# Kernel tuning notes

Hardware: AMD Instinct MI355X
Metric: run time of the kernel (lower is better)

The kernel has to match this reference:

```python
import jax, jax.numpy as jnp
import numpy as np

D = 1024       # d_model
H = 16         # nhead
HD = D // H    # head_dim = 64
FF = 4096      # dim_feedforward
EPS = 1e-5


def layer_norm(x, gamma, beta, eps=EPS):
    mu = jnp.mean(x, axis=-1, keepdims=True)
    var = jnp.var(x, axis=-1, keepdims=True)
    return (x - mu) * jax.lax.rsqrt(var + eps) * gamma + beta


def setup_inputs() -> dict:
    key = jax.random.key(0)
    ks = jax.random.split(key, 12)
    rn = lambda k, shape, s=0.02: (jax.random.normal(k, shape, jnp.float32) * s)
    return {
        "src": jax.random.normal(ks[0], (4, 2048, D), jnp.float32),
        "Wqkv": rn(ks[1], (D, 3 * D)),          # qkv_proj weight (bias=False), stored (in,out)
        "Wout": rn(ks[2], (D, D)),              # out_proj weight (bias=False)
        "W1": rn(ks[3], (D, FF)),               # linear1
        "b1": jnp.zeros((FF,), jnp.float32),
        "W2": rn(ks[4], (FF, D)),               # linear2
        "b2": jnp.zeros((D,), jnp.float32),
        "g1": jnp.ones((D,), jnp.float32),      # norm1 weight
        "be1": jnp.zeros((D,), jnp.float32),    # norm1 bias
        "g2": jnp.ones((D,), jnp.float32),      # norm2 weight
        "be2": jnp.zeros((D,), jnp.float32),    # norm2 bias
    }


def reference(src, Wqkv, Wout, W1, b1, W2, b2, g1, be1, g2, be2):
    B, S, _ = src.shape
    # --- self attention (naive/MATH-backend SDPA, post-norm, eval: dropout=0) ---
    qkv = src @ Wqkv                                  # [B,S,3D]
    qkv = qkv.reshape(B, S, 3, H, HD)
    q = qkv[:, :, 0].transpose(0, 2, 1, 3)            # [B,H,S,HD]
    k = qkv[:, :, 1].transpose(0, 2, 1, 3)
    v = qkv[:, :, 2].transpose(0, 2, 1, 3)
    scores = jnp.einsum("bhqd,bhkd->bhqk", q, k) / np.float32(np.sqrt(HD))  # [B,H,S,S]
    attn = jax.nn.softmax(scores, axis=-1)
    ctx = jnp.einsum("bhqk,bhkd->bhqd", attn, v)      # [B,H,S,HD]
    ctx = ctx.transpose(0, 2, 1, 3).reshape(B, S, D)  # [B,S,D]
    attn_out = ctx @ Wout
    # residual + norm1
    x = layer_norm(src + attn_out, g1, be1)
    # --- FFN ---
    ff = jax.nn.relu(x @ W1 + b1) @ W2 + b2
    # residual + norm2
    return layer_norm(x + ff, g2, be2)
```

## Files before the change

kernel.cpp:

```cpp
#include <hip/hip_runtime.h>
#include <hip/hip_bf16.h>


typedef __attribute__((ext_vector_type(8))) short          short8;
typedef __attribute__((ext_vector_type(8))) unsigned short ushort8;
typedef __attribute__((ext_vector_type(4))) float          f32x4;
typedef __attribute__((ext_vector_type(2))) unsigned int   uivec2;

__device__ __forceinline__ unsigned short f2bf(float f) {
    union { float f; unsigned int u; } v; v.f = f;
    unsigned int u = v.u;
    unsigned int r = (u + 0x7fffu + ((u >> 16) & 1u)) >> 16;
    return (unsigned short)r;
}

__device__ __forceinline__ float bf2f(unsigned short u) {
    union { unsigned int u; float f; } v; v.u = ((unsigned int)u) << 16;
    return v.f;
}

__device__ __forceinline__ unsigned int pack_bf16_trunc(float lo, float hi) {
    union { float f; unsigned int u; } a, b; a.f = lo; b.f = hi;
    return __builtin_amdgcn_perm(b.u, a.u, 0x07060302u);
}

__device__ __forceinline__ void async_load16(const void* g, void* l) {
    __builtin_amdgcn_global_load_lds(
        (const __attribute__((address_space(1))) void*)(unsigned long long)g,
        (__attribute__((address_space(3))) void*)(unsigned long long)l,
        16, 0, 0);
}

__device__ __forceinline__ void softmax_frag(const f32x4* s,
                                             short8& pf0, short8& pf1) {
    unsigned int aw[4], bw[4];
#pragma unroll
    for (int nt = 0; nt < 4; nt++) {
        float p0 = __builtin_amdgcn_exp2f(s[nt][0]);
        float p1 = __builtin_amdgcn_exp2f(s[nt][1]);
        float p2 = __builtin_amdgcn_exp2f(s[nt][2]);
        float p3 = __builtin_amdgcn_exp2f(s[nt][3]);
        aw[nt] = pack_bf16_trunc(p0, p1);
        bw[nt] = pack_bf16_trunc(p2, p3);
    }
    uivec2 rA = __builtin_amdgcn_permlane32_swap(aw[0], aw[1], false, false);
    uivec2 sA = __builtin_amdgcn_permlane32_swap(aw[2], aw[3], false, false);
    uivec2 rB = __builtin_amdgcn_permlane32_swap(bw[0], bw[1], false, false);
    uivec2 sB = __builtin_amdgcn_permlane32_swap(bw[2], bw[3], false, false);
    uivec2 tA = __builtin_amdgcn_permlane16_swap(rA.x, rA.y, false, false);
    uivec2 uA = __builtin_amdgcn_permlane16_swap(sA.x, sA.y, false, false);
    uivec2 tB = __builtin_amdgcn_permlane16_swap(rB.x, rB.y, false, false);
    uivec2 uB = __builtin_amdgcn_permlane16_swap(sB.x, sB.y, false, false);
    union { unsigned int w[4]; short8 v; } P0, P1;
    P0.w[0] = tA.x; P0.w[1] = tB.x; P0.w[2] = tA.y; P0.w[3] = tB.y;
    P1.w[0] = uA.x; P1.w[1] = uB.x; P1.w[2] = uA.y; P1.w[3] = uB.y;
    pf0 = P0.v;
    pf1 = P1.v;
}

__global__ __launch_bounds__(256) void cast_bf16_kernel(
    const float* __restrict__ x, unsigned short* __restrict__ y) {
    size_t i = ((size_t)blockIdx.x * 256 + threadIdx.x) * 4;
    float4 v = *(const float4*)(x + i);
    ushort4 o; o.x = f2bf(v.x); o.y = f2bf(v.y); o.z = f2bf(v.z); o.w = f2bf(v.w);
    *(ushort4*)(y + i) = o;
}

__global__ __launch_bounds__(256) void transpose_cast_kernel(
    const float* __restrict__ W, unsigned short* __restrict__ Wt, int K, int N) {
    __shared__ float tile[32][33];
    int n0 = blockIdx.x * 32, k0 = blockIdx.y * 32;
    int tx = threadIdx.x & 31, ty = threadIdx.x >> 5;
#pragma unroll
    for (int i = 0; i < 32; i += 8)
        tile[ty + i][tx] = W[(size_t)(k0 + ty + i) * N + n0 + tx];
    __syncthreads();
#pragma unroll
    for (int i = 0; i < 32; i += 8)
        Wt[(size_t)(n0 + ty + i) * K + k0 + tx] = f2bf(tile[tx][ty + i]);
}

template <int MODE>
__global__ __launch_bounds__(256) void gemm_bf16_kernel(
    const unsigned short* __restrict__ A, const unsigned short* __restrict__ Bt,
    int M, int N, int K, int Kstride,
    float* __restrict__ outF, unsigned short* __restrict__ outB,
    const float* __restrict__ bias,
    const float* __restrict__ resF, const unsigned short* __restrict__ resB,
    unsigned short* __restrict__ vtB) {
    __shared__ unsigned short As[2][128 * 32];
    __shared__ unsigned short Bs[2][128 * 32];

    const int t = threadIdx.x;
    const int m0 = blockIdx.x * 128, n0 = blockIdx.y * 128;
    const int koff = blockIdx.z * K;
    const int wid = t >> 6, lane = t & 63;
    const int wm = wid >> 1, wn = wid & 1;
    const int lr = lane & 15, quad = lane >> 4;

    const int srow = lane >> 2;
    const int sch  = ((lane & 3) ^ (srow & 3)) * 8;
    const unsigned short* Ag =
        A  + (size_t)(m0 + wid * 32 + srow) * Kstride + koff + sch;
    const unsigned short* Bg =
        Bt + (size_t)(n0 + wid * 32 + srow) * Kstride + koff + sch;
    const int wofs = (wid * 32) * 32;
    const size_t rstep = (size_t)16 * Kstride;

    const int axs = ((quad ^ (lr & 3))) * 8;
    f32x4 acc[4][4] = {};

    const int nK = K >> 5;
    async_load16(Ag,         &As[0][wofs]);
    async_load16(Ag + rstep, &As[0][wofs + 16 * 32]);
    async_load16(Bg,         &Bs[0][wofs]);
    async_load16(Bg + rstep, &Bs[0][wofs + 16 * 32]);

    for (int kt = 0; kt < nK; kt++) {
        const int cur = kt & 1, nxt = cur ^ 1;
        __syncthreads();
        if (kt + 1 < nK) {
            const int k1 = (kt + 1) * 32;
            async_load16(Ag + k1,         &As[nxt][wofs]);
            async_load16(Ag + k1 + rstep, &As[nxt][wofs + 16 * 32]);
            async_load16(Bg + k1,         &Bs[nxt][wofs]);
            async_load16(Bg + k1 + rstep, &Bs[nxt][wofs + 16 * 32]);
        }

        short8 af[4], bfr[4];
#pragma unroll
        for (int i = 0; i < 4; i++) {
            af[i]  = *(const short8*)&As[cur][(wm * 64 + i * 16 + lr) * 32 + axs];
            bfr[i] = *(const short8*)&Bs[cur][(wn * 64 + i * 16 + lr) * 32 + axs];
        }
#pragma unroll
        for (int mi = 0; mi < 4; mi++)
#pragma unroll
            for (int ni = 0; ni < 4; ni++)
                acc[mi][ni] = __builtin_amdgcn_mfma_f32_16x16x32_bf16(
                    af[mi], bfr[ni], acc[mi][ni], 0, 0, 0);
    }

    const float QSC = 0.18033688011112042f;
    float* pOut = (MODE == 5) ? outF + (size_t)blockIdx.z * M * N : outF;
    unsigned short* pOutB =
        (MODE == 8) ? outB + (size_t)blockIdx.z * M * N : outB;
#pragma unroll
    for (int mi = 0; mi < 4; mi++)
#pragma unroll
        for (int ni = 0; ni < 4; ni++) {
            const int col  = n0 + wn * 64 + ni * 16 + lr;
            const int row0 = m0 + wm * 64 + mi * 16 + quad * 4;
            if (MODE == 4 && col >= 2048) {
                int bb = row0 >> 11, ss = row0 & 2047, c = col - 2048;
                ushort4 ov;
                ov.x = f2bf(acc[mi][ni][0]); ov.y = f2bf(acc[mi][ni][1]);
                ov.z = f2bf(acc[mi][ni][2]); ov.w = f2bf(acc[mi][ni][3]);
                *(ushort4*)&vtB[((size_t)bb * 1024 + c) * 2048 + ss] = ov;
            } else {
#pragma unroll
                for (int r = 0; r < 4; r++) {
                    size_t idx = (size_t)(row0 + r) * N + col;
                    float v = acc[mi][ni][r];
                    if (MODE == 4) {
                        outB[idx] = f2bf(col < 1024 ? v * QSC : v);
                    } else if (MODE == 0) {
                        outB[idx] = f2bf(v);
                    } else if (MODE == 1) {
                        outF[idx] = v + resF[idx];
                    } else if (MODE == 2) {
                        v += bias[col];
                        outB[idx] = f2bf(v > 0.f ? v : 0.f);
                    } else if (MODE == 3) {
                        outF[idx] = v + bias[col] + bf2f(resB[idx]);
                    } else if (MODE == 7) {
                        outB[idx] = f2bf(v + bf2f(resB[idx]));
                    } else if (MODE == 8) {
                        pOutB[idx] = f2bf(v);
                    } else {
                        pOut[idx] = v;
                    }
                }
            }
        }
}

__global__ __launch_bounds__(256, 4) void attention_kernel(
    const unsigned short* __restrict__ qkv, const unsigned short* __restrict__ Vt,
    unsigned short* __restrict__ ctx) {
    __shared__ unsigned short Kbuf[2][64 * 64];
    __shared__ unsigned short Vbuf[2][64 * 64];

    const int qt = blockIdx.x, h = blockIdx.y, b = blockIdx.z;
    const int t = threadIdx.x, wid = t >> 6, lane = t & 63;
    const int lr = lane & 15, quad = lane >> 4;
    const int q0 = qt * 128 + wid * 32;

    size_t qbaseA = ((size_t)(b * 2048 + q0 + lr)) * 3072 + h * 64;
    size_t qbaseB = ((size_t)(b * 2048 + q0 + 16 + lr)) * 3072 + h * 64;
    short8 qfA0 = *(const short8*)(qkv + qbaseA + quad * 8);
    short8 qfA1 = *(const short8*)(qkv + qbaseA + 32 + quad * 8);
    short8 qfB0 = *(const short8*)(qkv + qbaseB + quad * 8);
    short8 qfB1 = *(const short8*)(qkv + qbaseB + 32 + quad * 8);

    const int srow = wid * 8 + (lane >> 3);
    const int sch  = ((lane & 7) ^ (srow & 7)) * 8;
    const unsigned short* Kg =
        qkv + (size_t)b * 2048 * 3072 + 1024 + h * 64 + (size_t)srow * 3072 + sch;
    const unsigned short* Vg =
        Vt + ((size_t)b * 1024 + h * 64 + srow) * 2048 + sch;
    unsigned short* KsB = (unsigned short*)&Kbuf[0][(wid * 8) * 64];
    unsigned short* VsB = (unsigned short*)&Vbuf[0][(wid * 8) * 64];
    const int bufstep = 64 * 64;

    short8 ones;
#pragma unroll
    for (int i = 0; i < 8; i++) ones[i] = (short)0x3F80;

    f32x4 oA[4] = {}, oB[4] = {};
    f32x4 laccA = {}, laccB = {};

#pragma unroll
    for (int half = 0; half < 2; half++) {
        async_load16(Kg + (size_t)(half * 32) * 3072, KsB + half * 32 * 64);
        async_load16(Vg + (size_t)(half * 32) * 2048, VsB + half * 32 * 64);
    }

    const int swz = lr & 7;

    for (int kt = 0; kt < 32; kt++) {
        const int cur = kt & 1, nxt = cur ^ 1;
        __syncthreads();
        if (kt + 1 < 32) {
#pragma unroll
            for (int half = 0; half < 2; half++) {
                async_load16(Kg + (size_t)((kt + 1) * 64 + half * 32) * 3072,
                             KsB + nxt * bufstep + half * 32 * 64);
                async_load16(Vg + (size_t)(half * 32) * 2048 + (kt + 1) * 64,
                             VsB + nxt * bufstep + half * 32 * 64);
            }
        }

        const unsigned short* Kc = &Kbuf[cur][0];
        const unsigned short* Vc = &Vbuf[cur][0];

        f32x4 sA[4] = {}, sB[4] = {};
#pragma unroll
        for (int nt = 0; nt < 4; nt++) {
            const unsigned short* krow = Kc + (nt * 16 + lr) * 64;
            short8 kf0 = *(const short8*)(krow + (quad ^ swz) * 8);
            short8 kf1 = *(const short8*)(krow + ((quad + 4) ^ swz) * 8);
            sA[nt] = __builtin_amdgcn_mfma_f32_16x16x32_bf16(kf0, qfA0, sA[nt], 0, 0, 0);
            sA[nt] = __builtin_amdgcn_mfma_f32_16x16x32_bf16(kf1, qfA1, sA[nt], 0, 0, 0);
            sB[nt] = __builtin_amdgcn_mfma_f32_16x16x32_bf16(kf0, qfB0, sB[nt], 0, 0, 0);
            sB[nt] = __builtin_amdgcn_mfma_f32_16x16x32_bf16(kf1, qfB1, sB[nt], 0, 0, 0);
        }

        short8 pfA0, pfA1, pfB0, pfB1;
        softmax_frag(sA, pfA0, pfA1);
        softmax_frag(sB, pfB0, pfB1);

#pragma unroll
        for (int nt = 0; nt < 4; nt++) {
            const unsigned short* vrow = Vc + (nt * 16 + lr) * 64;
            short8 vf0 = *(const short8*)(vrow + (quad ^ swz) * 8);
            short8 vf1 = *(const short8*)(vrow + ((quad + 4) ^ swz) * 8);
            oA[nt] = __builtin_amdgcn_mfma_f32_16x16x32_bf16(pfA0, vf0, oA[nt], 0, 0, 0);
            oA[nt] = __builtin_amdgcn_mfma_f32_16x16x32_bf16(pfA1, vf1, oA[nt], 0, 0, 0);
            oB[nt] = __builtin_amdgcn_mfma_f32_16x16x32_bf16(pfB0, vf0, oB[nt], 0, 0, 0);
            oB[nt] = __builtin_amdgcn_mfma_f32_16x16x32_bf16(pfB1, vf1, oB[nt], 0, 0, 0);
        }
        laccA = __builtin_amdgcn_mfma_f32_16x16x32_bf16(pfA0, ones, laccA, 0, 0, 0);
        laccA = __builtin_amdgcn_mfma_f32_16x16x32_bf16(pfA1, ones, laccA, 0, 0, 0);
        laccB = __builtin_amdgcn_mfma_f32_16x16x32_bf16(pfB0, ones, laccB, 0, 0, 0);
        laccB = __builtin_amdgcn_mfma_f32_16x16x32_bf16(pfB1, ones, laccB, 0, 0, 0);
    }

#pragma unroll
    for (int r = 0; r < 4; r++) {
        float liA = 1.f / laccA[r];
        float liB = 1.f / laccB[r];
        int qA = q0 + quad * 4 + r;
        int qB = q0 + 16 + quad * 4 + r;
#pragma unroll
        for (int nt = 0; nt < 4; nt++) {
            ctx[((size_t)(b * 2048 + qA)) * 1024 + h * 64 + nt * 16 + lr] =
                f2bf(oA[nt][r] * liA);
            ctx[((size_t)(b * 2048 + qB)) * 1024 + h * 64 + nt * 16 + lr] =
                f2bf(oB[nt][r] * liB);
        }
    }
}

__global__ __launch_bounds__(256) void layernorm_bf_kernel(
    const unsigned short* __restrict__ x, const float* __restrict__ g,
    const float* __restrict__ be, unsigned short* __restrict__ yB) {
    const int row = blockIdx.x, t = threadIdx.x;
    ushort4 xb = *(const ushort4*)(x + (size_t)row * 1024 + t * 4);
    float4 v;
    v.x = bf2f(xb.x); v.y = bf2f(xb.y); v.z = bf2f(xb.z); v.w = bf2f(xb.w);
    float s  = v.x + v.y + v.z + v.w;
    float sq = v.x * v.x + v.y * v.y + v.z * v.z + v.w * v.w;
#pragma unroll
    for (int d = 1; d < 64; d <<= 1) {
        s  += __shfl_xor(s, d, 64);
        sq += __shfl_xor(sq, d, 64);
    }
    __shared__ float sh[8];
    int wid = t >> 6, lane = t & 63;
    if (lane == 0) { sh[wid] = s; sh[4 + wid] = sq; }
    __syncthreads();
    s  = sh[0] + sh[1] + sh[2] + sh[3];
    sq = sh[4] + sh[5] + sh[6] + sh[7];
    float mu  = s * (1.f / 1024.f);
    float var = sq * (1.f / 1024.f) - mu * mu;
    float rstd = rsqrtf(var + 1e-5f);
    float4 gv = *(const float4*)(g + t * 4);
    float4 bv = *(const float4*)(be + t * 4);
    ushort4 o;
    o.x = f2bf((v.x - mu) * rstd * gv.x + bv.x);
    o.y = f2bf((v.y - mu) * rstd * gv.y + bv.y);
    o.z = f2bf((v.z - mu) * rstd * gv.z + bv.z);
    o.w = f2bf((v.w - mu) * rstd * gv.w + bv.w);
    *(ushort4*)(yB + (size_t)row * 1024 + t * 4) = o;
}

__global__ __launch_bounds__(256) void layernorm_sum2_kernel(
    const unsigned short* __restrict__ p0, const unsigned short* __restrict__ p1,
    const float* __restrict__ bias, const unsigned short* __restrict__ res,
    const float* __restrict__ g, const float* __restrict__ be,
    float* __restrict__ out) {
    const int row = blockIdx.x, t = threadIdx.x;
    const size_t base = (size_t)row * 1024 + t * 4;
    ushort4 a = *(const ushort4*)(p0 + base);
    ushort4 b = *(const ushort4*)(p1 + base);
    float4 bi = *(const float4*)(bias + t * 4);
    ushort4 rb = *(const ushort4*)(res + base);
    float4 v;
    v.x = bf2f(a.x) + bf2f(b.x) + bi.x + bf2f(rb.x);
    v.y = bf2f(a.y) + bf2f(b.y) + bi.y + bf2f(rb.y);
    v.z = bf2f(a.z) + bf2f(b.z) + bi.z + bf2f(rb.z);
    v.w = bf2f(a.w) + bf2f(b.w) + bi.w + bf2f(rb.w);
    float s  = v.x + v.y + v.z + v.w;
    float sq = v.x * v.x + v.y * v.y + v.z * v.z + v.w * v.w;
#pragma unroll
    for (int d = 1; d < 64; d <<= 1) {
        s  += __shfl_xor(s, d, 64);
        sq += __shfl_xor(sq, d, 64);
    }
    __shared__ float sh[8];
    int wid = t >> 6, lane = t & 63;
    if (lane == 0) { sh[wid] = s; sh[4 + wid] = sq; }
    __syncthreads();
    s  = sh[0] + sh[1] + sh[2] + sh[3];
    sq = sh[4] + sh[5] + sh[6] + sh[7];
    float mu  = s * (1.f / 1024.f);
    float var = sq * (1.f / 1024.f) - mu * mu;
    float rstd = rsqrtf(var + 1e-5f);
    float4 gv = *(const float4*)(g + t * 4);
    float4 bv = *(const float4*)(be + t * 4);
    float4 y;
    y.x = (v.x - mu) * rstd * gv.x + bv.x;
    y.y = (v.y - mu) * rstd * gv.y + bv.y;
    y.z = (v.z - mu) * rstd * gv.z + bv.z;
    y.w = (v.w - mu) * rstd * gv.w + bv.w;
    *(float4*)(out + base) = y;
}

extern "C" void kernel_launch(void* const* d_in, const int* in_sizes, int n_in,
                              void* d_out, int out_size, void* d_ws, size_t ws_size,
                              hipStream_t stream) {
    const float* src  = (const float*)d_in[0];
    const float* Wqkv = (const float*)d_in[1];
    const float* Wout = (const float*)d_in[2];
    const float* W1   = (const float*)d_in[3];
    const float* b1   = (const float*)d_in[4];
    const float* W2   = (const float*)d_in[5];
    const float* b2   = (const float*)d_in[6];
    const float* g1   = (const float*)d_in[7];
    const float* be1  = (const float*)d_in[8];
    const float* g2   = (const float*)d_in[9];
    const float* be2  = (const float*)d_in[10];
    float* out = (float*)d_out;

    const size_t NT = 8192;
    char* ws = (char*)d_ws;
    unsigned short* src_bf = (unsigned short*)ws; ws += NT * 1024 * 2;
    unsigned short* Wqkv_t = (unsigned short*)ws; ws += (size_t)3072 * 1024 * 2;
    unsigned short* Wout_t = (unsigned short*)ws; ws += (size_t)1024 * 1024 * 2;
    unsigned short* W1_t   = (unsigned short*)ws; ws += (size_t)4096 * 1024 * 2;
    unsigned short* W2_t   = (unsigned short*)ws; ws += (size_t)1024 * 4096 * 2;
    unsigned short* qkv_bf = (unsigned short*)ws; ws += NT * 3072 * 2;
    unsigned short* ctx_bf = (unsigned short*)ws; ws += NT * 1024 * 2;
    unsigned short* x1_bf  = (unsigned short*)ws; ws += NT * 1024 * 2;
    unsigned short* y1_bf  = (unsigned short*)ws; ws += NT * 1024 * 2;
    unsigned short* h_bf   = (unsigned short*)ws; ws += NT * 4096 * 2;
    unsigned short* Vt = h_bf;
    unsigned short* part = qkv_bf;

    cast_bf16_kernel<<<8192, 256, 0, stream>>>(src, src_bf);
    transpose_cast_kernel<<<dim3(96, 32), 256, 0, stream>>>(Wqkv, Wqkv_t, 1024, 3072);
    transpose_cast_kernel<<<dim3(32, 32), 256, 0, stream>>>(Wout, Wout_t, 1024, 1024);
    transpose_cast_kernel<<<dim3(128, 32), 256, 0, stream>>>(W1, W1_t, 1024, 4096);
    transpose_cast_kernel<<<dim3(32, 128), 256, 0, stream>>>(W2, W2_t, 4096, 1024);

    gemm_bf16_kernel<4><<<dim3(64, 24), 256, 0, stream>>>(
        src_bf, Wqkv_t, 8192, 3072, 1024, 1024,
        nullptr, qkv_bf, nullptr, nullptr, nullptr, Vt);
    attention_kernel<<<dim3(16, 16, 4), 256, 0, stream>>>(qkv_bf, Vt, ctx_bf);
    gemm_bf16_kernel<7><<<dim3(64, 8), 256, 0, stream>>>(
        ctx_bf, Wout_t, 8192, 1024, 1024, 1024,
        nullptr, x1_bf, nullptr, nullptr, src_bf, nullptr);
    layernorm_bf_kernel<<<8192, 256, 0, stream>>>(x1_bf, g1, be1, y1_bf);
    gemm_bf16_kernel<2><<<dim3(64, 32), 256, 0, stream>>>(
        y1_bf, W1_t, 8192, 4096, 1024, 1024,
        nullptr, h_bf, b1, nullptr, nullptr, nullptr);
    gemm_bf16_kernel<8><<<dim3(64, 8, 2), 256, 0, stream>>>(
        h_bf, W2_t, 8192, 1024, 2048, 4096,
        nullptr, part, nullptr, nullptr, nullptr, nullptr);
    layernorm_sum2_kernel<<<8192, 256, 0, stream>>>(
        part, part + NT * 1024, b2, y1_bf, g2, be2, out);
}
```

Before: 513.7 us.

## Merge prep kernels and drop split-K in FFN2 with fused bias/residual epilogue

Folds the src cast and four weight transpose-casts into one prep kernel, removing four launches. The second FFN GEMM stops splitting K into two halves with bf16 partials. It now runs the full K=4096 on a 64x8 grid and adds bias and residual in its epilogue, so the final layernorm reads a single bf16 tensor. This saves a partial-sum round trip and launches, but halves the FFN2 grid's parallelism (512 blocks), which may underfill the GPU.

```diff
diff --git a/kernel.cpp b/kernel.cpp
--- a/kernel.cpp
+++ b/kernel.cpp
@@ -58,18 +58,9 @@
     pf1 = P1.v;
 }
 
-__global__ __launch_bounds__(256) void cast_bf16_kernel(
-    const float* __restrict__ x, unsigned short* __restrict__ y) {
-    size_t i = ((size_t)blockIdx.x * 256 + threadIdx.x) * 4;
-    float4 v = *(const float4*)(x + i);
-    ushort4 o; o.x = f2bf(v.x); o.y = f2bf(v.y); o.z = f2bf(v.z); o.w = f2bf(v.w);
-    *(ushort4*)(y + i) = o;
-}
-
-__global__ __launch_bounds__(256) void transpose_cast_kernel(
-    const float* __restrict__ W, unsigned short* __restrict__ Wt, int K, int N) {
-    __shared__ float tile[32][33];
-    int n0 = blockIdx.x * 32, k0 = blockIdx.y * 32;
+__device__ __forceinline__ void transpose_tile32(
+    const float* __restrict__ W, unsigned short* __restrict__ Wt,
+    int K, int N, int n0, int k0, float (*tile)[33]) {
     int tx = threadIdx.x & 31, ty = threadIdx.x >> 5;
 #pragma unroll
     for (int i = 0; i < 32; i += 8)
@@ -78,6 +69,35 @@
 #pragma unroll
     for (int i = 0; i < 32; i += 8)
         Wt[(size_t)(n0 + ty + i) * K + k0 + tx] = f2bf(tile[tx][ty + i]);
+}
+
+__global__ __launch_bounds__(256) void prep_kernel(
+    const float* __restrict__ src, unsigned short* __restrict__ src_bf,
+    const float* __restrict__ Wqkv, unsigned short* __restrict__ Wqkv_t,
+    const float* __restrict__ Wout, unsigned short* __restrict__ Wout_t,
+    const float* __restrict__ W1, unsigned short* __restrict__ W1_t,
+    const float* __restrict__ W2, unsigned short* __restrict__ W2_t) {
+    __shared__ float tile[32][33];
+    const int bid = blockIdx.x;
+    if (bid < 8192) {
+        size_t i = ((size_t)bid * 256 + threadIdx.x) * 4;
+        float4 v = *(const float4*)(src + i);
+        ushort4 o;
+        o.x = f2bf(v.x); o.y = f2bf(v.y); o.z = f2bf(v.z); o.w = f2bf(v.w);
+        *(ushort4*)(src_bf + i) = o;
+    } else if (bid < 11264) {
+        int r = bid - 8192;
+        transpose_tile32(Wqkv, Wqkv_t, 1024, 3072, (r % 96) * 32, (r / 96) * 32, tile);
+    } else if (bid < 12288) {
+        int r = bid - 11264;
+        transpose_tile32(Wout, Wout_t, 1024, 1024, (r % 32) * 32, (r / 32) * 32, tile);
+    } else if (bid < 16384) {
+        int r = bid - 12288;
+        transpose_tile32(W1, W1_t, 1024, 4096, (r % 128) * 32, (r / 128) * 32, tile);
+    } else {
+        int r = bid - 16384;
+        transpose_tile32(W2, W2_t, 4096, 1024, (r % 32) * 32, (r / 32) * 32, tile);
+    }
 }
 
 template <int MODE>
@@ -142,9 +162,6 @@
     }
 
     const float QSC = 0.18033688011112042f;
-    float* pOut = (MODE == 5) ? outF + (size_t)blockIdx.z * M * N : outF;
-    unsigned short* pOutB =
-        (MODE == 8) ? outB + (size_t)blockIdx.z * M * N : outB;
 #pragma unroll
     for (int mi = 0; mi < 4; mi++)
 #pragma unroll
@@ -171,14 +188,10 @@
                     } else if (MODE == 2) {
                         v += bias[col];
                         outB[idx] = f2bf(v > 0.f ? v : 0.f);
-                    } else if (MODE == 3) {
-                        outF[idx] = v + bias[col] + bf2f(resB[idx]);
                     } else if (MODE == 7) {
                         outB[idx] = f2bf(v + bf2f(resB[idx]));
-                    } else if (MODE == 8) {
-                        pOutB[idx] = f2bf(v);
-                    } else {
-                        pOut[idx] = v;
+                    } else if (MODE == 9) {
+                        outB[idx] = f2bf(v + bias[col] + bf2f(resB[idx]));
                     }
                 }
             }
@@ -292,55 +305,15 @@
     }
 }
 
+template <int OUTMODE>
 __global__ __launch_bounds__(256) void layernorm_bf_kernel(
     const unsigned short* __restrict__ x, const float* __restrict__ g,
-    const float* __restrict__ be, unsigned short* __restrict__ yB) {
+    const float* __restrict__ be, float* __restrict__ yF,
+    unsigned short* __restrict__ yB) {
     const int row = blockIdx.x, t = threadIdx.x;
     ushort4 xb = *(const ushort4*)(x + (size_t)row * 1024 + t * 4);
     float4 v;
     v.x = bf2f(xb.x); v.y = bf2f(xb.y); v.z = bf2f(xb.z); v.w = bf2f(xb.w);
-    float s  = v.x + v.y + v.z + v.w;
-    float sq = v.x * v.x + v.y * v.y + v.z * v.z + v.w * v.w;
-#pragma unroll
-    for (int d = 1; d < 64; d <<= 1) {
-        s  += __shfl_xor(s, d, 64);
-        sq += __shfl_xor(sq, d, 64);
-    }
-    __shared__ float sh[8];
-    int wid = t >> 6, lane = t & 63;
-    if (lane == 0) { sh[wid] = s; sh[4 + wid] = sq; }
-    __syncthreads();
-    s  = sh[0] + sh[1] + sh[2] + sh[3];
-    sq = sh[4] + sh[5] + sh[6] + sh[7];
-    float mu  = s * (1.f / 1024.f);
-    float var = sq * (1.f / 1024.f) - mu * mu;
-    float rstd = rsqrtf(var + 1e-5f);
-    float4 gv = *(const float4*)(g + t * 4);
-    float4 bv = *(const float4*)(be + t * 4);
-    ushort4 o;
-    o.x = f2bf((v.x - mu) * rstd * gv.x + bv.x);
-    o.y = f2bf((v.y - mu) * rstd * gv.y + bv.y);
-    o.z = f2bf((v.z - mu) * rstd * gv.z + bv.z);
-    o.w = f2bf((v.w - mu) * rstd * gv.w + bv.w);
-    *(ushort4*)(yB + (size_t)row * 1024 + t * 4) = o;
-}
-
-__global__ __launch_bounds__(256) void layernorm_sum2_kernel(
-    const unsigned short* __restrict__ p0, const unsigned short* __restrict__ p1,
-    const float* __restrict__ bias, const unsigned short* __restrict__ res,
-    const float* __restrict__ g, const float* __restrict__ be,
-    float* __restrict__ out) {
-    const int row = blockIdx.x, t = threadIdx.x;
-    const size_t base = (size_t)row * 1024 + t * 4;
-    ushort4 a = *(const ushort4*)(p0 + base);
-    ushort4 b = *(const ushort4*)(p1 + base);
-    float4 bi = *(const float4*)(bias + t * 4);
-    ushort4 rb = *(const ushort4*)(res + base);
-    float4 v;
-    v.x = bf2f(a.x) + bf2f(b.x) + bi.x + bf2f(rb.x);
-    v.y = bf2f(a.y) + bf2f(b.y) + bi.y + bf2f(rb.y);
-    v.z = bf2f(a.z) + bf2f(b.z) + bi.z + bf2f(rb.z);
-    v.w = bf2f(a.w) + bf2f(b.w) + bi.w + bf2f(rb.w);
     float s  = v.x + v.y + v.z + v.w;
     float sq = v.x * v.x + v.y * v.y + v.z * v.z + v.w * v.w;
 #pragma unroll
@@ -364,7 +337,13 @@
     y.y = (v.y - mu) * rstd * gv.y + bv.y;
     y.z = (v.z - mu) * rstd * gv.z + bv.z;
     y.w = (v.w - mu) * rstd * gv.w + bv.w;
-    *(float4*)(out + base) = y;
+    if (OUTMODE == 0) {
+        *(float4*)(yF + (size_t)row * 1024 + t * 4) = y;
+    } else {
+        ushort4 o;
+        o.x = f2bf(y.x); o.y = f2bf(y.y); o.z = f2bf(y.z); o.w = f2bf(y.w);
+        *(ushort4*)(yB + (size_t)row * 1024 + t * 4) = o;
+    }
 }
 
 extern "C" void kernel_launch(void* const* d_in, const int* in_sizes, int n_in,
@@ -396,13 +375,10 @@
     unsigned short* y1_bf  = (unsigned short*)ws; ws += NT * 1024 * 2;
     unsigned short* h_bf   = (unsigned short*)ws; ws += NT * 4096 * 2;
     unsigned short* Vt = h_bf;
-    unsigned short* part = qkv_bf;
-
-    cast_bf16_kernel<<<8192, 256, 0, stream>>>(src, src_bf);
-    transpose_cast_kernel<<<dim3(96, 32), 256, 0, stream>>>(Wqkv, Wqkv_t, 1024, 3072);
-    transpose_cast_kernel<<<dim3(32, 32), 256, 0, stream>>>(Wout, Wout_t, 1024, 1024);
-    transpose_cast_kernel<<<dim3(128, 32), 256, 0, stream>>>(W1, W1_t, 1024, 4096);
-    transpose_cast_kernel<<<dim3(32, 128), 256, 0, stream>>>(W2, W2_t, 4096, 1024);
+    unsigned short* x2_bf = qkv_bf;
+
+    prep_kernel<<<20480, 256, 0, stream>>>(
+        src, src_bf, Wqkv, Wqkv_t, Wout, Wout_t, W1, W1_t, W2, W2_t);
 
     gemm_bf16_kernel<4><<<dim3(64, 24), 256, 0, stream>>>(
         src_bf, Wqkv_t, 8192, 3072, 1024, 1024,
@@ -411,13 +387,14 @@
     gemm_bf16_kernel<7><<<dim3(64, 8), 256, 0, stream>>>(
         ctx_bf, Wout_t, 8192, 1024, 1024, 1024,
         nullptr, x1_bf, nullptr, nullptr, src_bf, nullptr);
-    layernorm_bf_kernel<<<8192, 256, 0, stream>>>(x1_bf, g1, be1, y1_bf);
+    layernorm_bf_kernel<1><<<8192, 256, 0, stream>>>(
+        x1_bf, g1, be1, nullptr, y1_bf);
     gemm_bf16_kernel<2><<<dim3(64, 32), 256, 0, stream>>>(
         y1_bf, W1_t, 8192, 4096, 1024, 1024,
         nullptr, h_bf, b1, nullptr, nullptr, nullptr);
-    gemm_bf16_kernel<8><<<dim3(64, 8, 2), 256, 0, stream>>>(
-        h_bf, W2_t, 8192, 1024, 2048, 4096,
-        nullptr, part, nullptr, nullptr, nullptr, nullptr);
-    layernorm_sum2_kernel<<<8192, 256, 0, stream>>>(
-        part, part + NT * 1024, b2, y1_bf, g2, be2, out);
-}
+    gemm_bf16_kernel<9><<<dim3(64, 8), 256, 0, stream>>>(
+        h_bf, W2_t, 8192, 1024, 4096, 4096,
+        nullptr, x2_bf, b2, nullptr, y1_bf, nullptr);
+    layernorm_bf_kernel<0><<<8192, 256, 0, stream>>>(
+        x2_bf, g2, be2, out, nullptr);
+}
```

Result: faster. 484.4 us (-5.7%).
